# Kernel optimization log

Hardware: AMD Instinct MI355X
Metric: run time of the kernel (lower is better)

The kernel has to match this reference:

```python
import jax, jax.numpy as jnp
import numpy as np

B, S, D, E, K = 4, 4096, 2048, 64, 2


def setup_inputs() -> dict:
    key = jax.random.key(0)
    kx, kwg, kwn, kn = jax.random.split(key, 4)
    scale = 1.0 / np.sqrt(D)
    return {
        "x": jax.random.normal(kx, (B, S, D), dtype=jnp.float32),
        "Wg": jax.random.normal(kwg, (E, D), dtype=jnp.float32) * scale,
        "bg": jnp.zeros((E,), dtype=jnp.float32),
        "Wn": jax.random.normal(kwn, (E, D), dtype=jnp.float32) * scale,
        "bn": jnp.zeros((E,), dtype=jnp.float32),
        "noise": jax.random.normal(kn, (B, S, E), dtype=jnp.float32),
    }


def reference(x, Wg, bg, Wn, bn, noise):
    # gate / noise projections: [B,S,D] @ [D,E] -> [B,S,E]
    gate_logits = jnp.einsum("bsd,ed->bse", x, Wg) + bg
    noise_std = jax.nn.softplus(jnp.einsum("bsd,ed->bse", x, Wn) + bn)
    noisy_logits = gate_logits + noise * noise_std  # training-mode path

    # top-k over experts, then scatter back with -inf elsewhere
    flat = noisy_logits.reshape(-1, E)  # [T, E], T = B*S
    top_vals, top_idx = jax.lax.top_k(flat, K)  # [T, K]
    T = flat.shape[0]
    neg_inf = jnp.full((T, E), -jnp.inf, dtype=flat.dtype)
    full_logits = neg_inf.at[jnp.arange(T)[:, None], top_idx].set(top_vals)

    gate_probs = jax.nn.softmax(full_logits, axis=-1).reshape(B, S, E)
    top_k_indices = top_idx.reshape(B, S, K)
    return gate_probs, top_k_indices
```

## Files before the change

### kernel.cpp

```cpp
#include <hip/hip_runtime.h>
#include <math.h>
#include <stdint.h>

#define D_ 2048
#define E_ 64
#define T_ 16384

#define BM 64
#define BK 64
#define KTILES 32
#define ABUF_B 16384
#define BBUF_B 32768
#define BUF_B (ABUF_B + BBUF_B)
#define CT_STRIDE 132

typedef _Float16 h8 __attribute__((ext_vector_type(8)));
typedef float f4v __attribute__((ext_vector_type(4)));

__device__ __forceinline__ void split2(const float4& a, const float4& b,
                                       h8& h, h8& m) {
    const float xe[8] = {a.x, a.y, a.z, a.w, b.x, b.y, b.z, b.w};
#pragma unroll
    for (int i = 0; i < 8; ++i) {
        const _Float16 hh_ = (_Float16)xe[i];
        const float r = (xe[i] - (float)hh_) * 1024.0f;
        h[i] = hh_;
        m[i] = (_Float16)r;
    }
}

__device__ __forceinline__ void gload16(const void* g, void* l) {
    __builtin_amdgcn_global_load_lds(
        (const __attribute__((address_space(1))) uint32_t*)g,
        (__attribute__((address_space(3))) uint32_t*)l, 16, 0, 0);
}

__device__ __forceinline__ void topk_epilogue(float g, float nl, float nz,
                                              int lane, size_t tg,
                                              float* __restrict__ out_probs,
                                              float* __restrict__ out_idx) {
    const float sp = fmaxf(nl, 0.f) + log1pf(expf(-fabsf(nl)));
    const float noisy = g + nz * sp;

    float v = noisy;
    int idx = lane;
#pragma unroll
    for (int off = 32; off > 0; off >>= 1) {
        const float ov = __shfl_xor(v, off);
        const int oi = __shfl_xor(idx, off);
        if (ov > v || (ov == v && oi < idx)) { v = ov; idx = oi; }
    }
    const float v1 = v;
    const int i1 = idx;
    v = (lane == i1) ? -INFINITY : noisy;
    idx = lane;
#pragma unroll
    for (int off = 32; off > 0; off >>= 1) {
        const float ov = __shfl_xor(v, off);
        const int oi = __shfl_xor(idx, off);
        if (ov > v || (ov == v && oi < idx)) { v = ov; idx = oi; }
    }
    const float v2 = v;
    const int i2 = idx;

    const float e2 = expf(v2 - v1);
    const float denom = 1.f + e2;
    const float p = (lane == i1) ? (1.f / denom)
                                 : ((lane == i2) ? (e2 / denom) : 0.f);
    out_probs[tg * E_ + lane] = p;
    if (lane == 0) {
        out_idx[tg * 2 + 0] = (float)i1;
        out_idx[tg * 2 + 1] = (float)i2;
    }
}

__global__ void w_split_kernel(const float* __restrict__ Wg,
                               const float* __restrict__ Wn,
                               h8* __restrict__ wsp) {
    const int idx = blockIdx.x * blockDim.x + threadIdx.x;
    const int lane = idx & 63;
    const int s = (idx >> 6) & 63;
    const int f = idx >> 12;
    const int n = f * 16 + (lane & 15);
    const int k0 = s * 32 + ((lane >> 4) << 3);
    const float* src = (n < 64) ? &Wg[(size_t)n * D_ + k0]
                                : &Wn[(size_t)(n - 64) * D_ + k0];
    h8 hv, mv;
#pragma unroll
    for (int i = 0; i < 8; ++i) {
        const float w = src[i];
        const _Float16 wh = (_Float16)w;
        const float r = (w - (float)wh) * 1024.0f;
        hv[i] = wh;
        mv[i] = (_Float16)r;
    }
    wsp[0 * 32768 + idx] = hv;
    wsp[1 * 32768 + idx] = mv;
}

__launch_bounds__(512)
__global__ void gemm_topk_kernel(const float* __restrict__ x,
                                 const h8* __restrict__ wsp,
                                 const float* __restrict__ bg,
                                 const float* __restrict__ bn,
                                 const float* __restrict__ noise,
                                 float* __restrict__ out_probs,
                                 float* __restrict__ out_idx) {
    __shared__ __align__(16) char smem[2 * BUF_B];
    const int tid = threadIdx.x;
    const int lane = tid & 63;
    const int wv = tid >> 6;
    const int wm = wv >> 2;
    const int wn = wv & 3;
    const int block_m0 = blockIdx.x * BM;
    const char* wb = (const char*)wsp;

    const int sfrag = tid >> 7;
    const int sks = (tid >> 6) & 1;
    const int sl = tid & 63;
    const int srow = sfrag * 16 + (sl & 15);
    const int schunk = sks * 4 + (sl >> 4);
    const float* asrc = x + (size_t)(block_m0 + srow) * D_ + schunk * 8;
    const int aw_hi = ((0 * 4 + sfrag) * 2 + sks) * 1024 + sl * 16;
    const int aw_mid = ((1 * 4 + sfrag) * 2 + sks) * 1024 + sl * 16;

    f4v hh[2][2] = {}, cx[2][2] = {}, mm[2][2] = {};

    auto STAGE_B = [&](int t, int b) {
        char* Bb = smem + b * BUF_B + ABUF_B;
#pragma unroll
        for (int p = 0; p < 2; ++p)
#pragma unroll
            for (int ks = 0; ks < 2; ++ks)
                gload16(wb + ((size_t)(p * 32768 + wv * 4096 + (t * 2 + ks) * 64 + lane)) * 16,
                        Bb + ((p * 8 + wv) * 2 + ks) * 1024 + lane * 16);
    };
    auto ALOAD = [&](int t, float4& ra, float4& rb) {
        ra = *(const float4*)(asrc + t * BK);
        rb = *(const float4*)(asrc + t * BK + 4);
    };
    auto ASPLIT = [&](const float4& ra, const float4& rb, int b) {
        h8 hv, mv;
        split2(ra, rb, hv, mv);
        char* Ab = smem + b * BUF_B;
        *(h8*)(Ab + aw_hi) = hv;
        *(h8*)(Ab + aw_mid) = mv;
    };
    auto COMPUTE = [&](int b) {
        const char* Ab = smem + b * BUF_B;
        const char* Bb = Ab + ABUF_B;
#pragma unroll
        for (int ks = 0; ks < 2; ++ks) {
            h8 ah[2], am[2], bh[2], bm[2];
#pragma unroll
            for (int mi = 0; mi < 2; ++mi) {
                const int mf = wm * 2 + mi;
                ah[mi] = *(const h8*)(Ab + ((0 * 4 + mf) * 2 + ks) * 1024 + lane * 16);
                am[mi] = *(const h8*)(Ab + ((1 * 4 + mf) * 2 + ks) * 1024 + lane * 16);
            }
#pragma unroll
            for (int nf = 0; nf < 2; ++nf) {
                const int f = wn * 2 + nf;
                bh[nf] = *(const h8*)(Bb + ((0 * 8 + f) * 2 + ks) * 1024 + lane * 16);
                bm[nf] = *(const h8*)(Bb + ((1 * 8 + f) * 2 + ks) * 1024 + lane * 16);
            }
#define MF(A, B, C) C = __builtin_amdgcn_mfma_f32_16x16x32_f16(A, B, C, 0, 0, 0)
#pragma unroll
            for (int mi = 0; mi < 2; ++mi)
#pragma unroll
                for (int nf = 0; nf < 2; ++nf) {
                    MF(ah[mi], bh[nf], hh[mi][nf]);
                    MF(ah[mi], bm[nf], cx[mi][nf]);
                    MF(am[mi], bh[nf], cx[mi][nf]);
                    MF(am[mi], bm[nf], mm[mi][nf]);
                }
#undef MF
        }
    };

    float4 ra0, rb0, ra1, rb1;
    ALOAD(0, ra0, rb0);
    STAGE_B(0, 0);
    ASPLIT(ra0, rb0, 0);
    ALOAD(1, ra0, rb0);
    __syncthreads();

#pragma unroll 1
    for (int i = 0; i < KTILES / 2; ++i) {
        const int t = 2 * i;
        STAGE_B(t + 1, 1);
        if (t + 2 < KTILES) ALOAD(t + 2, ra1, rb1);
        COMPUTE(0);
        ASPLIT(ra0, rb0, 1);
        __syncthreads();
        if (t + 2 < KTILES) STAGE_B(t + 2, 0);
        if (t + 3 < KTILES) ALOAD(t + 3, ra0, rb0);
        COMPUTE(1);
        if (t + 2 < KTILES) ASPLIT(ra1, rb1, 0);
        __syncthreads();
    }

    float* Ct = (float*)smem;
    {
        const float S1 = 1.0f / 1024.0f;
        const float S2 = S1 * S1;
        const int arow = lane & 15;
        const int ko4 = (lane >> 4) * 4;
#pragma unroll
        for (int mi = 0; mi < 2; ++mi)
#pragma unroll
            for (int nf = 0; nf < 2; ++nf) {
                const int col = wn * 32 + nf * 16 + arow;
#pragma unroll
                for (int r = 0; r < 4; ++r) {
                    const int row = wm * 32 + mi * 16 + ko4 + r;
                    Ct[row * CT_STRIDE + col] =
                        hh[mi][nf][r] + cx[mi][nf][r] * S1 + mm[mi][nf][r] * S2;
                }
            }
    }
    __syncthreads();

    const float my_bg = bg[lane];
    const float my_bn = bn[lane];
#pragma unroll 1
    for (int tt = 0; tt < 8; ++tt) {
        const int tl = wv * 8 + tt;
        const size_t tg = (size_t)block_m0 + tl;
        const float g = Ct[tl * CT_STRIDE + lane] + my_bg;
        const float nl = Ct[tl * CT_STRIDE + 64 + lane] + my_bn;
        const float nz = noise[tg * E_ + lane];
        topk_epilogue(g, nl, nz, lane, tg, out_probs, out_idx);
    }
}

#define FBM 64
#define FBK 32
#define XS_STRIDE 68
#define WS_STRIDE 132
#define FCT_STRIDE 132

__launch_bounds__(256)
__global__ void noisy_topk_f32_kernel(const float* __restrict__ x,
                                      const float* __restrict__ Wg,
                                      const float* __restrict__ bg,
                                      const float* __restrict__ Wn,
                                      const float* __restrict__ bn,
                                      const float* __restrict__ noise,
                                      float* __restrict__ out_probs,
                                      float* __restrict__ out_idx) {
    __shared__ float smem[FBM * FCT_STRIDE];
    float* Xs = smem;
    float* Ws = smem + FBK * XS_STRIDE;

    const int tid = threadIdx.x;
    const int block_m0 = blockIdx.x * FBM;
    const int n0 = (tid & 31) * 4;
    const int m0 = (tid >> 5) * 8;

    float acc[8][4];
#pragma unroll
    for (int i = 0; i < 8; ++i)
#pragma unroll
        for (int j = 0; j < 4; ++j) acc[i][j] = 0.f;

    const int sj = tid & 7;
    const int sr = tid >> 3;

    for (int k0 = 0; k0 < D_; k0 += FBK) {
        __syncthreads();
#pragma unroll
        for (int it = 0; it < 2; ++it) {
            const int m = sr + it * 32;
            const float4 v = *reinterpret_cast<const float4*>(
                &x[(size_t)(block_m0 + m) * D_ + k0 + 4 * sj]);
            Xs[(4 * sj + 0) * XS_STRIDE + m] = v.x;
            Xs[(4 * sj + 1) * XS_STRIDE + m] = v.y;
            Xs[(4 * sj + 2) * XS_STRIDE + m] = v.z;
            Xs[(4 * sj + 3) * XS_STRIDE + m] = v.w;
        }
#pragma unroll
        for (int it = 0; it < 4; ++it) {
            const int n = sr + it * 32;
            const float* wrow = (n < 64) ? &Wg[(size_t)n * D_] : &Wn[(size_t)(n - 64) * D_];
            const float4 v = *reinterpret_cast<const float4*>(&wrow[k0 + 4 * sj]);
            Ws[(4 * sj + 0) * WS_STRIDE + n] = v.x;
            Ws[(4 * sj + 1) * WS_STRIDE + n] = v.y;
            Ws[(4 * sj + 2) * WS_STRIDE + n] = v.z;
            Ws[(4 * sj + 3) * WS_STRIDE + n] = v.w;
        }
        __syncthreads();
#pragma unroll
        for (int k = 0; k < FBK; ++k) {
            const float4 a0 = *reinterpret_cast<const float4*>(&Xs[k * XS_STRIDE + m0]);
            const float4 a1 = *reinterpret_cast<const float4*>(&Xs[k * XS_STRIDE + m0 + 4]);
            const float4 b4 = *reinterpret_cast<const float4*>(&Ws[k * WS_STRIDE + n0]);
            const float am[8] = {a0.x, a0.y, a0.z, a0.w, a1.x, a1.y, a1.z, a1.w};
            const float bb[4] = {b4.x, b4.y, b4.z, b4.w};
#pragma unroll
            for (int i = 0; i < 8; ++i)
#pragma unroll
                for (int j = 0; j < 4; ++j)
                    acc[i][j] = fmaf(am[i], bb[j], acc[i][j]);
        }
    }

    __syncthreads();
    float* Ct = smem;
#pragma unroll
    for (int i = 0; i < 8; ++i)
#pragma unroll
        for (int j = 0; j < 4; ++j)
            Ct[(m0 + i) * FCT_STRIDE + n0 + j] = acc[i][j];
    __syncthreads();

    const int wave = tid >> 6;
    const int lane = tid & 63;
    const float my_bg = bg[lane];
    const float my_bn = bn[lane];
#pragma unroll 1
    for (int tt = 0; tt < 16; ++tt) {
        const int tl = wave * 16 + tt;
        const size_t tg = (size_t)block_m0 + tl;
        const float g = Ct[tl * FCT_STRIDE + lane] + my_bg;
        const float nl = Ct[tl * FCT_STRIDE + 64 + lane] + my_bn;
        const float nz = noise[tg * E_ + lane];
        topk_epilogue(g, nl, nz, lane, tg, out_probs, out_idx);
    }
}

extern "C" void kernel_launch(void* const* d_in, const int* in_sizes, int n_in,
                              void* d_out, int out_size, void* d_ws, size_t ws_size,
                              hipStream_t stream) {
    const float* x = (const float*)d_in[0];
    const float* Wg = (const float*)d_in[1];
    const float* bg = (const float*)d_in[2];
    const float* Wn = (const float*)d_in[3];
    const float* bn = (const float*)d_in[4];
    const float* noise = (const float*)d_in[5];
    float* out_probs = (float*)d_out;
    float* out_idx = out_probs + (size_t)T_ * E_;

    const size_t WSP_BYTES = (size_t)2 * 32768 * 16;
    if (ws_size >= WSP_BYTES) {
        h8* wsp = (h8*)d_ws;
        hipLaunchKernelGGL(w_split_kernel, dim3(128), dim3(256), 0, stream, Wg, Wn, wsp);
        hipLaunchKernelGGL(gemm_topk_kernel, dim3(T_ / BM), dim3(512), 0, stream,
                           x, wsp, bg, bn, noise, out_probs, out_idx);
    } else {
        hipLaunchKernelGGL(noisy_topk_f32_kernel, dim3(T_ / FBM), dim3(256), 0, stream,
                           x, Wg, bg, Wn, bn, noise, out_probs, out_idx);
    }
}
```

Measured before the change: 59.62 us.

## Halve GEMM row tile to 32 tokens per block for more blocks

Result: slower. 61.11 us (+2.5%).

```diff
diff --git a/kernel.cpp b/kernel.cpp
--- a/kernel.cpp
+++ b/kernel.cpp
@@ -6,10 +6,10 @@
 #define E_ 64
 #define T_ 16384
 
-#define BM 64
+#define BM 32
 #define BK 64
 #define KTILES 32
-#define ABUF_B 16384
+#define ABUF_B 8192
 #define BBUF_B 32768
 #define BUF_B (ABUF_B + BBUF_B)
 #define CT_STRIDE 132
@@ -98,7 +98,7 @@
     wsp[1 * 32768 + idx] = mv;
 }
 
-__launch_bounds__(512)
+__launch_bounds__(512, 4)
 __global__ void gemm_topk_kernel(const float* __restrict__ x,
                                  const h8* __restrict__ wsp,
                                  const float* __restrict__ bg,
@@ -115,16 +115,16 @@
     const int block_m0 = blockIdx.x * BM;
     const char* wb = (const char*)wsp;
 
-    const int sfrag = tid >> 7;
+    const int sfrag = (tid >> 7) & 1;
     const int sks = (tid >> 6) & 1;
     const int sl = tid & 63;
     const int srow = sfrag * 16 + (sl & 15);
     const int schunk = sks * 4 + (sl >> 4);
     const float* asrc = x + (size_t)(block_m0 + srow) * D_ + schunk * 8;
-    const int aw_hi = ((0 * 4 + sfrag) * 2 + sks) * 1024 + sl * 16;
-    const int aw_mid = ((1 * 4 + sfrag) * 2 + sks) * 1024 + sl * 16;
-
-    f4v hh[2][2] = {}, cx[2][2] = {}, mm[2][2] = {};
+    const int aw_hi = ((0 * 2 + sfrag) * 2 + sks) * 1024 + sl * 16;
+    const int aw_mid = ((1 * 2 + sfrag) * 2 + sks) * 1024 + sl * 16;
+
+    f4v hh[2] = {}, cx[2] = {}, mm[2] = {};
 
     auto STAGE_B = [&](int t, int b) {
         char* Bb = smem + b * BUF_B + ABUF_B;
@@ -136,28 +136,28 @@
                         Bb + ((p * 8 + wv) * 2 + ks) * 1024 + lane * 16);
     };
     auto ALOAD = [&](int t, float4& ra, float4& rb) {
-        ra = *(const float4*)(asrc + t * BK);
-        rb = *(const float4*)(asrc + t * BK + 4);
+        if (tid < 256) {
+            ra = *(const float4*)(asrc + t * BK);
+            rb = *(const float4*)(asrc + t * BK + 4);
+        }
     };
     auto ASPLIT = [&](const float4& ra, const float4& rb, int b) {
-        h8 hv, mv;
-        split2(ra, rb, hv, mv);
-        char* Ab = smem + b * BUF_B;
-        *(h8*)(Ab + aw_hi) = hv;
-        *(h8*)(Ab + aw_mid) = mv;
+        if (tid < 256) {
+            h8 hv, mv;
+            split2(ra, rb, hv, mv);
+            char* Ab = smem + b * BUF_B;
+            *(h8*)(Ab + aw_hi) = hv;
+            *(h8*)(Ab + aw_mid) = mv;
+        }
     };
     auto COMPUTE = [&](int b) {
         const char* Ab = smem + b * BUF_B;
         const char* Bb = Ab + ABUF_B;
 #pragma unroll
         for (int ks = 0; ks < 2; ++ks) {
-            h8 ah[2], am[2], bh[2], bm[2];
-#pragma unroll
-            for (int mi = 0; mi < 2; ++mi) {
-                const int mf = wm * 2 + mi;
-                ah[mi] = *(const h8*)(Ab + ((0 * 4 + mf) * 2 + ks) * 1024 + lane * 16);
-                am[mi] = *(const h8*)(Ab + ((1 * 4 + mf) * 2 + ks) * 1024 + lane * 16);
-            }
+            h8 ah, am, bh[2], bm[2];
+            ah = *(const h8*)(Ab + ((0 * 2 + wm) * 2 + ks) * 1024 + lane * 16);
+            am = *(const h8*)(Ab + ((1 * 2 + wm) * 2 + ks) * 1024 + lane * 16);
 #pragma unroll
             for (int nf = 0; nf < 2; ++nf) {
                 const int f = wn * 2 + nf;
@@ -166,19 +166,17 @@
             }
 #define MF(A, B, C) C = __builtin_amdgcn_mfma_f32_16x16x32_f16(A, B, C, 0, 0, 0)
 #pragma unroll
-            for (int mi = 0; mi < 2; ++mi)
-#pragma unroll
-                for (int nf = 0; nf < 2; ++nf) {
-                    MF(ah[mi], bh[nf], hh[mi][nf]);
-                    MF(ah[mi], bm[nf], cx[mi][nf]);
-                    MF(am[mi], bh[nf], cx[mi][nf]);
-                    MF(am[mi], bm[nf], mm[mi][nf]);
-                }
+            for (int nf = 0; nf < 2; ++nf) {
+                MF(ah, bh[nf], hh[nf]);
+                MF(ah, bm[nf], cx[nf]);
+                MF(am, bh[nf], cx[nf]);
+                MF(am, bm[nf], mm[nf]);
+            }
 #undef MF
         }
     };
 
-    float4 ra0, rb0, ra1, rb1;
+    float4 ra0{}, rb0{}, ra1{}, rb1{};
     ALOAD(0, ra0, rb0);
     STAGE_B(0, 0);
     ASPLIT(ra0, rb0, 0);
@@ -207,25 +205,23 @@
         const int arow = lane & 15;
         const int ko4 = (lane >> 4) * 4;
 #pragma unroll
-        for (int mi = 0; mi < 2; ++mi)
-#pragma unroll
-            for (int nf = 0; nf < 2; ++nf) {
-                const int col = wn * 32 + nf * 16 + arow;
-#pragma unroll
-                for (int r = 0; r < 4; ++r) {
-                    const int row = wm * 32 + mi * 16 + ko4 + r;
-                    Ct[row * CT_STRIDE + col] =
-                        hh[mi][nf][r] + cx[mi][nf][r] * S1 + mm[mi][nf][r] * S2;
-                }
+        for (int nf = 0; nf < 2; ++nf) {
+            const int col = wn * 32 + nf * 16 + arow;
+#pragma unroll
+            for (int r = 0; r < 4; ++r) {
+                const int row = wm * 16 + ko4 + r;
+                Ct[row * CT_STRIDE + col] =
+                    hh[nf][r] + cx[nf][r] * S1 + mm[nf][r] * S2;
             }
+        }
     }
     __syncthreads();
 
     const float my_bg = bg[lane];
     const float my_bn = bn[lane];
 #pragma unroll 1
-    for (int tt = 0; tt < 8; ++tt) {
-        const int tl = wv * 8 + tt;
+    for (int tt = 0; tt < 4; ++tt) {
+        const int tl = wv * 4 + tt;
         const size_t tg = (size_t)block_m0 + tl;
         const float g = Ct[tl * CT_STRIDE + lane] + my_bg;
         const float nl = Ct[tl * CT_STRIDE + 64 + lane] + my_bn;
```
